# Kernel optimization log

Measured on AMD Instinct MI355X. Metric: run time of the kernel, lower is better.

The kernel has to match this reference:

```python
import jax, jax.numpy as jnp
import numpy as np

THRESHOLD = 0.9
EPS = 1e-12


def setup_inputs() -> dict:
    key = jax.random.key(0)
    ks = jax.random.split(key, 7)
    B, D_in, H1, H2, D_out = 8192, 256, 512, 256, 64
    # torch Linear default init ~ U(-1/sqrt(fan_in), 1/sqrt(fan_in)); randn scaled is fine as a stand-in
    def lin(k, out_f, in_f):
        return jax.random.normal(k, (out_f, in_f), dtype=jnp.float32) / np.sqrt(in_f)
    return {
        "x": jax.random.normal(ks[0], (B, D_in), dtype=jnp.float32),
        "W1": lin(ks[1], H1, D_in),
        "b1": jax.random.normal(ks[2], (H1,), dtype=jnp.float32) * 0.01,
        "W2": lin(ks[3], H2, H1),
        "b2": jax.random.normal(ks[4], (H2,), dtype=jnp.float32) * 0.01,
        "W3": lin(ks[5], D_out, H2),
        "b3": jax.random.normal(ks[6], (D_out,), dtype=jnp.float32) * 0.01,
    }


def reference(x, W1, b1, W2, b2, W3, b3):
    # MLP: Linear -> Tanh -> Linear -> Tanh -> Linear (no tanh on last)
    h1 = jnp.tanh(x @ W1.T + b1)          # [B, 512]
    h2 = jnp.tanh(h1 @ W2.T + b2)         # [B, 256]
    out = h2 @ W3.T + b3                  # [B, 64]

    # Pairwise state fidelity: (normalized dot)^2, thresholded adjacency (diag excluded)
    norms = jnp.linalg.norm(out, axis=-1, keepdims=True)  # [B, 1]
    normed = out / (norms + EPS)
    fid = (normed @ normed.T) ** 2                         # [B, B]
    adj = (fid >= THRESHOLD).astype(out.dtype)
    B = out.shape[0]
    adj = adj * (1.0 - jnp.eye(B, dtype=out.dtype))        # no self-edges (i < j pairs only)

    return adj @ out                                       # [B, 64]
```

## Files before the change

### kernel.cpp

```cpp
#include <hip/hip_runtime.h>
#include <hip/hip_bf16.h>
#include <math.h>

#define B_ROWS 8192
#define D_IN   256
#define H1_DIM 512
#define H2_DIM 256
#define D_OUT  64
#define EPSF   1e-12f
#define THRESH 0.9f
#define BAND_LO 0.89f
#define BAND_HI 0.91f

typedef __attribute__((ext_vector_type(8))) short short8;
typedef __attribute__((ext_vector_type(4))) float f32x4;

__device__ inline float tanh_fast(float xx) {
  const float ax = fabsf(xx);
  const float t = __expf(-2.0f * ax);
  const float r = (1.0f - t) / (1.0f + t);
  return xx < 0.0f ? -r : r;
}

__device__ inline void splitf8(float4 a, float4 b, short8& h, short8& m) {
  float v[8] = {a.x, a.y, a.z, a.w, b.x, b.y, b.z, b.w};
  short h8[8], m8[8];
#pragma unroll
  for (int e = 0; e < 8; ++e) {
    __hip_bfloat16 hb = __float2bfloat16(v[e]);
    float hf = __bfloat162float(hb);
    __hip_bfloat16 mb = __float2bfloat16(v[e] - hf);
    h8[e] = *(short*)&hb;
    m8[e] = *(short*)&mb;
  }
  h = *(short8*)h8;
  m = *(short8*)m8;
}

__device__ inline void rd8_swz(const float* buf, int S, int row, int kl,
                               float4& a, float4& b) {
  const int xr = (row & 7) << 2;
  a = *(const float4*)&buf[(row * S + kl) ^ xr];
  b = *(const float4*)&buf[(row * S + kl + 4) ^ xr];
}

__device__ inline void pack8(const float* __restrict__ src, short* __restrict__ dh,
                             short* __restrict__ dm, int t, int C, int lgq) {
  const int lane = t & 63;
  const int g = t >> 6;
  const int q = g & ((1 << lgq) - 1);
  const int I = g >> lgq;
  const int row = I * 16 + (lane & 15);
  const int k0 = q * 32 + ((lane >> 4) << 3);
  const float* p = src + (size_t)row * C + k0;
  short8 hh, mm;
  splitf8(*(const float4*)p, *(const float4*)(p + 4), hh, mm);
  *(short8*)(dh + (size_t)t * 8) = hh;
  *(short8*)(dm + (size_t)t * 8) = mm;
}

__global__ __launch_bounds__(256)
void wpack(const float* __restrict__ W1, const float* __restrict__ W2,
           const float* __restrict__ W3,
           short* w1h, short* w1m, short* w2h, short* w2m,
           short* w3h, short* w3m) {
  const int b = blockIdx.x, tid = threadIdx.x;
  if (b < 64)        pack8(W1, w1h, w1m, b * 256 + tid, 256, 3);
  else if (b < 128)  pack8(W2, w2h, w2m, (b - 64) * 256 + tid, 512, 4);
  else               pack8(W3, w3h, w3m, (b - 128) * 256 + tid, 256, 3);
}

__global__ __launch_bounds__(512, 4)
void fused_mlp16(const float* __restrict__ x,
                 const short* __restrict__ w1h, const short* __restrict__ w1m,
                 const float* __restrict__ b1,
                 const short* __restrict__ w2h, const short* __restrict__ w2m,
                 const float* __restrict__ b2,
                 const short* __restrict__ w3h, const short* __restrict__ w3m,
                 const float* __restrict__ b3,
                 float* __restrict__ out, short* __restrict__ vph,
                 short* __restrict__ vpm, float* __restrict__ res) {
  __shared__ __align__(16) char smem[49152];
  short* xph   = (short*)smem;
  short* xpm   = (short*)(smem + 8192);
  float* wbuf1 = (float*)smem;
  float* wbuf3 = (float*)smem;
  short* h1h   = (short*)(smem + 16384);
  short* h1m   = (short*)(smem + 32768);
  float* wbuf2 = (float*)(smem + 16384);
  short* h2ph  = (short*)(smem + 32768);
  short* h2pm  = (short*)(smem + 40960);
  __shared__ float nsum[16];
  __shared__ float invn[16];

  const int tid = threadIdx.x;
  const int wave = tid >> 6, lane = tid & 63;
  const int r0 = blockIdx.x * 16;
  const int col16 = lane & 15;
  const int rbase = (lane >> 4) << 2;

  if (tid < 256) {
    float4* rz = (float4*)(res + (size_t)r0 * D_OUT);
    rz[tid] = make_float4(0.f, 0.f, 0.f, 0.f);
  }

  {
    const int lu = tid & 63, q = tid >> 6;
    const float* p = x + (size_t)(r0 + (lu & 15)) * D_IN + q * 32 + ((lu >> 4) << 3);
    short8 hh, mm;
    splitf8(*(const float4*)p, *(const float4*)(p + 4), hh, mm);
    const int off = (q * 64 + lu) * 8;
    *(short8*)(xph + off) = hh;
    *(short8*)(xpm + off) = mm;
  }
  __syncthreads();

  f32x4 acc1[4];
#pragma unroll
  for (int jj = 0; jj < 4; ++jj) acc1[jj] = (f32x4){0.f, 0.f, 0.f, 0.f};
#pragma unroll 4
  for (int q = 0; q < 8; ++q) {
    const int aoff = (q * 64 + lane) * 8;
    const short8 Ah = *(const short8*)(xph + aoff);
    const short8 Am = *(const short8*)(xpm + aoff);
#pragma unroll
    for (int jj = 0; jj < 4; ++jj) {
      const int boff = (((wave * 4 + jj) * 8 + q) * 64 + lane) * 8;
      const short8 Bh = *(const short8*)(w1h + boff);
      const short8 Bm = *(const short8*)(w1m + boff);
      acc1[jj] = __builtin_amdgcn_mfma_f32_16x16x32_bf16(Ah, Bh, acc1[jj], 0, 0, 0);
      acc1[jj] = __builtin_amdgcn_mfma_f32_16x16x32_bf16(Ah, Bm, acc1[jj], 0, 0, 0);
      acc1[jj] = __builtin_amdgcn_mfma_f32_16x16x32_bf16(Am, Bh, acc1[jj], 0, 0, 0);
    }
  }
  __syncthreads();

  float bv1[4];
#pragma unroll
  for (int jj = 0; jj < 4; ++jj) bv1[jj] = b1[(wave * 4 + jj) * 16 + col16];
#pragma unroll
  for (int h = 0; h < 2; ++h) {
    if ((wave >> 2) == h) {
#pragma unroll
      for (int jj = 0; jj < 4; ++jj)
#pragma unroll
        for (int r = 0; r < 4; ++r) {
          const int row = rbase + r;
          const int col = ((wave & 3) * 4 + jj) * 16 + col16;
          wbuf1[(row * 256 + col) ^ ((row & 7) << 2)] = tanh_fast(acc1[jj][r] + bv1[jj]);
        }
    }
    __syncthreads();
    {
      const int lu = tid & 63, ql = tid >> 6;
      const int row = lu & 15, kl = ql * 32 + ((lu >> 4) << 3);
      float4 a, b;
      rd8_swz(wbuf1, 256, row, kl, a, b);
      short8 hh, mm;
      splitf8(a, b, hh, mm);
      const int off = ((h * 8 + ql) * 64 + lu) * 8;
      *(short8*)(h1h + off) = hh;
      *(short8*)(h1m + off) = mm;
    }
    __syncthreads();
  }

  f32x4 acc2[2];
#pragma unroll
  for (int jj = 0; jj < 2; ++jj) acc2[jj] = (f32x4){0.f, 0.f, 0.f, 0.f};
#pragma unroll 4
  for (int q = 0; q < 16; ++q) {
    const int aoff = (q * 64 + lane) * 8;
    const short8 Ah = *(const short8*)(h1h + aoff);
    const short8 Am = *(const short8*)(h1m + aoff);
#pragma unroll
    for (int jj = 0; jj < 2; ++jj) {
      const int boff = (((wave * 2 + jj) * 16 + q) * 64 + lane) * 8;
      const short8 Bh = *(const short8*)(w2h + boff);
      const short8 Bm = *(const short8*)(w2m + boff);
      acc2[jj] = __builtin_amdgcn_mfma_f32_16x16x32_bf16(Ah, Bh, acc2[jj], 0, 0, 0);
      acc2[jj] = __builtin_amdgcn_mfma_f32_16x16x32_bf16(Ah, Bm, acc2[jj], 0, 0, 0);
      acc2[jj] = __builtin_amdgcn_mfma_f32_16x16x32_bf16(Am, Bh, acc2[jj], 0, 0, 0);
    }
  }
  __syncthreads();

  {
    float bv2[2];
#pragma unroll
    for (int jj = 0; jj < 2; ++jj) bv2[jj] = b2[(wave * 2 + jj) * 16 + col16];
#pragma unroll
    for (int jj = 0; jj < 2; ++jj)
#pragma unroll
      for (int r = 0; r < 4; ++r) {
        const int row = rbase + r;
        const int col = (wave * 2 + jj) * 16 + col16;
        wbuf2[(row * 256 + col) ^ ((row & 7) << 2)] = tanh_fast(acc2[jj][r] + bv2[jj]);
      }
  }
  __syncthreads();
  {
    const int lu = tid & 63, ql = tid >> 6;
    const int row = lu & 15, kl = ql * 32 + ((lu >> 4) << 3);
    float4 a, b;
    rd8_swz(wbuf2, 256, row, kl, a, b);
    short8 hh, mm;
    splitf8(a, b, hh, mm);
    const int off = (ql * 64 + lu) * 8;
    *(short8*)(h2ph + off) = hh;
    *(short8*)(h2pm + off) = mm;
  }
  __syncthreads();

  if (wave < 4) {
    f32x4 acc3 = (f32x4){0.f, 0.f, 0.f, 0.f};
#pragma unroll 4
    for (int q = 0; q < 8; ++q) {
      const int aoff = (q * 64 + lane) * 8;
      const short8 Ah = *(const short8*)(h2ph + aoff);
      const short8 Am = *(const short8*)(h2pm + aoff);
      const int boff = ((wave * 8 + q) * 64 + lane) * 8;
      const short8 Bh = *(const short8*)(w3h + boff);
      const short8 Bm = *(const short8*)(w3m + boff);
      acc3 = __builtin_amdgcn_mfma_f32_16x16x32_bf16(Ah, Bh, acc3, 0, 0, 0);
      acc3 = __builtin_amdgcn_mfma_f32_16x16x32_bf16(Ah, Bm, acc3, 0, 0, 0);
      acc3 = __builtin_amdgcn_mfma_f32_16x16x32_bf16(Am, Bh, acc3, 0, 0, 0);
    }
    const float bv3 = b3[wave * 16 + col16];
#pragma unroll
    for (int r = 0; r < 4; ++r) {
      const int row = rbase + r;
      const int col = wave * 16 + col16;
      wbuf3[(row * 64 + col) ^ ((row & 7) << 2)] = acc3[r] + bv3;
    }
  }
  __syncthreads();

  if (tid < 256) {
    const int row = tid >> 4, c4 = (tid & 15) * 4;
    const float4 a = *(const float4*)&wbuf3[(row * 64 + c4) ^ ((row & 7) << 2)];
    float s = a.x * a.x + a.y * a.y + a.z * a.z + a.w * a.w;
    s += __shfl_xor(s, 1, 64);
    s += __shfl_xor(s, 2, 64);
    s += __shfl_xor(s, 4, 64);
    s += __shfl_xor(s, 8, 64);
    if ((tid & 15) == 0) nsum[row] = s;
  }
  __syncthreads();
  if (tid < 16) invn[tid] = 1.0f / (sqrtf(nsum[tid]) + EPSF);
  __syncthreads();

  if (tid < 256) {
    const int row = tid >> 4, c4 = (tid & 15) * 4;
    *(float4*)(out + (size_t)(r0 + row) * D_OUT + c4) =
        *(const float4*)&wbuf3[(row * 64 + c4) ^ ((row & 7) << 2)];
  }
  if (tid < 128) {
    const int lu = tid & 63, ql = tid >> 6;
    const int row = lu & 15, kl = ql * 32 + ((lu >> 4) << 3);
    const float sc = invn[row];
    float4 a, b;
    rd8_swz(wbuf3, 64, row, kl, a, b);
    a.x *= sc; a.y *= sc; a.z *= sc; a.w *= sc;
    b.x *= sc; b.y *= sc; b.z *= sc; b.w *= sc;
    short8 hh, mm;
    splitf8(a, b, hh, mm);
    const size_t off = (((size_t)blockIdx.x * 2 + ql) * 64 + lu) * 8;
    *(short8*)(vph + off) = hh;
    *(short8*)(vpm + off) = mm;
  }
}

__global__ __launch_bounds__(256, 2)
void gram_accum(const short* __restrict__ vph, const short* __restrict__ vpm,
                const float* __restrict__ out, float* __restrict__ res) {
  __shared__ __align__(16) short lAh[8 * 1024];
  const int tid = threadIdx.x;
  const int wave = tid >> 6, lane = tid & 63;

  const int t = blockIdx.x;
  int I = (int)((129.0f - sqrtf(16641.0f - 8.0f * (float)t)) * 0.5f);
  if (I < 0) I = 0;
  while (64 * (I + 1) - ((I + 1) * I) / 2 <= t) ++I;
  while (64 * I - (I * (I - 1)) / 2 > t) --I;
  const int Jc = I + (t - (64 * I - (I * (I - 1)) / 2));
  const int i0 = I * 128;
  const int j0c = Jc * 128;

  {
    const size_t base = (size_t)I * 8192;
#pragma unroll
    for (int u = 0; u < 4; ++u) {
      const int item = wave * 4 + u;
      __builtin_amdgcn_global_load_lds(
          (const __attribute__((address_space(1))) void*)(vph + base + item * 512 + lane * 8),
          (__attribute__((address_space(3))) void*)(lAh + item * 512), 16, 0, 0);
    }
  }
  __syncthreads();

  short8 Ah[8][2];
#pragma unroll
  for (int it = 0; it < 8; ++it)
#pragma unroll
    for (int q = 0; q < 2; ++q)
      Ah[it][q] = *(const short8*)(lAh + it * 1024 + q * 512 + lane * 8);

#pragma unroll
  for (int tt = 0; tt < 2; ++tt) {
    const int jt = wave * 2 + tt;
    const int j0 = j0c + jt * 16;
    const short* jb_h = vph + (size_t)(j0 >> 4) * 1024;
    short8 Bh0 = *(const short8*)(jb_h + lane * 8);
    short8 Bh1 = *(const short8*)(jb_h + 512 + lane * 8);

    f32x4 g[8];
#pragma unroll
    for (int it = 0; it < 8; ++it) g[it] = (f32x4){0.f, 0.f, 0.f, 0.f};
#pragma unroll
    for (int it = 0; it < 8; ++it) g[it] = __builtin_amdgcn_mfma_f32_16x16x32_bf16(Ah[it][0], Bh0, g[it], 0, 0, 0);
#pragma unroll
    for (int it = 0; it < 8; ++it) g[it] = __builtin_amdgcn_mfma_f32_16x16x32_bf16(Ah[it][1], Bh1, g[it], 0, 0, 0);

    bool band = false;
#pragma unroll
    for (int it = 0; it < 8; ++it)
#pragma unroll
      for (int r = 0; r < 4; ++r) {
        const float f = g[it][r] * g[it][r];
        band = band || (f > BAND_LO && f < BAND_HI);
      }
    if (__any(band)) {
      const short* jb_m = vpm + (size_t)(j0 >> 4) * 1024;
      short8 Bm0 = *(const short8*)(jb_m + lane * 8);
      short8 Bm1 = *(const short8*)(jb_m + 512 + lane * 8);
#pragma unroll
      for (int it = 0; it < 8; ++it) g[it] = __builtin_amdgcn_mfma_f32_16x16x32_bf16(Ah[it][0], Bm0, g[it], 0, 0, 0);
#pragma unroll
      for (int it = 0; it < 8; ++it) g[it] = __builtin_amdgcn_mfma_f32_16x16x32_bf16(Ah[it][1], Bm1, g[it], 0, 0, 0);
#pragma unroll
      for (int it = 0; it < 8; ++it) {
        const size_t abase = (size_t)((i0 >> 4) + it) * 1024;
        short8 Am0 = *(const short8*)(vpm + abase + lane * 8);
        short8 Am1 = *(const short8*)(vpm + abase + 512 + lane * 8);
        g[it] = __builtin_amdgcn_mfma_f32_16x16x32_bf16(Am0, Bh0, g[it], 0, 0, 0);
        g[it] = __builtin_amdgcn_mfma_f32_16x16x32_bf16(Am1, Bh1, g[it], 0, 0, 0);
      }
    }

    const int jl = j0 + (lane & 15);
#pragma unroll
    for (int it = 0; it < 8; ++it)
#pragma unroll
      for (int r = 0; r < 4; ++r) {
        const int il = i0 + it * 16 + (lane >> 4) * 4 + r;
        unsigned long long m =
            __ballot((g[it][r] * g[it][r] >= THRESH) && (il < jl));
        while (m) {
          const int s = __builtin_ctzll(m);
          m &= m - 1;
          const int js = j0 + (s & 15);
          const int is = i0 + it * 16 + ((s >> 4) << 2) + r;
          atomicAdd(res + (size_t)is * D_OUT + lane, out[(size_t)js * D_OUT + lane]);
          atomicAdd(res + (size_t)js * D_OUT + lane, out[(size_t)is * D_OUT + lane]);
        }
      }
  }
}

#define MB (1024 * 1024)
#define KB 1024

extern "C" void kernel_launch(void* const* d_in, const int* in_sizes, int n_in,
                              void* d_out, int out_size, void* d_ws, size_t ws_size,
                              hipStream_t stream) {
  const float* x  = (const float*)d_in[0];
  const float* W1 = (const float*)d_in[1];
  const float* b1 = (const float*)d_in[2];
  const float* W2 = (const float*)d_in[3];
  const float* b2 = (const float*)d_in[4];
  const float* W3 = (const float*)d_in[5];
  const float* b3 = (const float*)d_in[6];
  float* res = (float*)d_out;

  char* ws = (char*)d_ws;
  float* out = (float*)(ws);
  short* vph = (short*)(ws + 2 * MB);
  short* vpm = (short*)(ws + 3 * MB);
  short* w1h = (short*)(ws + 4 * MB);
  short* w1m = (short*)(ws + 4 * MB + 256 * KB);
  short* w2h = (short*)(ws + 4 * MB + 512 * KB);
  short* w2m = (short*)(ws + 4 * MB + 768 * KB);
  short* w3h = (short*)(ws + 5 * MB);
  short* w3m = (short*)(ws + 5 * MB + 32 * KB);

  wpack<<<136, 256, 0, stream>>>(W1, W2, W3, w1h, w1m, w2h, w2m, w3h, w3m);
  fused_mlp16<<<512, 512, 0, stream>>>(x, w1h, w1m, b1, w2h, w2m, b2,
                                       w3h, w3m, b3, out, vph, vpm, res);
  gram_accum<<<dim3(2080), 256, 0, stream>>>(vph, vpm, out, res);
}
```

Baseline: 117.9 us.

## Process 32 rows per MLP block and stream Gram A-fragments from LDS

```diff
diff --git a/kernel.cpp b/kernel.cpp
--- a/kernel.cpp
+++ b/kernel.cpp
@@ -70,8 +70,8 @@
   else               pack8(W3, w3h, w3m, (b - 128) * 256 + tid, 256, 3);
 }
 
-__global__ __launch_bounds__(512, 4)
-void fused_mlp16(const float* __restrict__ x,
+__global__ __launch_bounds__(512, 2)
+void fused_mlp32(const float* __restrict__ x,
                  const short* __restrict__ w1h, const short* __restrict__ w1m,
                  const float* __restrict__ b1,
                  const short* __restrict__ w2h, const short* __restrict__ w2m,
@@ -80,57 +80,67 @@
                  const float* __restrict__ b3,
                  float* __restrict__ out, short* __restrict__ vph,
                  short* __restrict__ vpm, float* __restrict__ res) {
-  __shared__ __align__(16) char smem[49152];
+  __shared__ __align__(16) char smem[98304];
   short* xph   = (short*)smem;
-  short* xpm   = (short*)(smem + 8192);
-  float* wbuf1 = (float*)smem;
-  float* wbuf3 = (float*)smem;
-  short* h1h   = (short*)(smem + 16384);
-  short* h1m   = (short*)(smem + 32768);
-  float* wbuf2 = (float*)(smem + 16384);
+  short* xpm   = (short*)(smem + 16384);
+  float* wbuf  = (float*)smem;
+  short* h1h   = (short*)(smem + 32768);
+  short* h1m   = (short*)(smem + 65536);
   short* h2ph  = (short*)(smem + 32768);
-  short* h2pm  = (short*)(smem + 40960);
-  __shared__ float nsum[16];
-  __shared__ float invn[16];
+  short* h2pm  = (short*)(smem + 49152);
+  __shared__ float nsum[32];
+  __shared__ float invn[32];
 
   const int tid = threadIdx.x;
   const int wave = tid >> 6, lane = tid & 63;
-  const int r0 = blockIdx.x * 16;
+  const int r0 = blockIdx.x * 32;
   const int col16 = lane & 15;
   const int rbase = (lane >> 4) << 2;
 
-  if (tid < 256) {
+  {
     float4* rz = (float4*)(res + (size_t)r0 * D_OUT);
     rz[tid] = make_float4(0.f, 0.f, 0.f, 0.f);
   }
 
-  {
-    const int lu = tid & 63, q = tid >> 6;
-    const float* p = x + (size_t)(r0 + (lu & 15)) * D_IN + q * 32 + ((lu >> 4) << 3);
+#pragma unroll
+  for (int uu = 0; uu < 2; ++uu) {
+    const int u = tid + uu * 512;
+    const int lu = u & 63, g = u >> 6;
+    const int q = g & 7, it = g >> 3;
+    const float* p = x + (size_t)(r0 + it * 16 + (lu & 15)) * D_IN + q * 32 + ((lu >> 4) << 3);
     short8 hh, mm;
     splitf8(*(const float4*)p, *(const float4*)(p + 4), hh, mm);
-    const int off = (q * 64 + lu) * 8;
+    const int off = ((it * 8 + q) * 64 + lu) * 8;
     *(short8*)(xph + off) = hh;
     *(short8*)(xpm + off) = mm;
   }
   __syncthreads();
 
-  f32x4 acc1[4];
-#pragma unroll
-  for (int jj = 0; jj < 4; ++jj) acc1[jj] = (f32x4){0.f, 0.f, 0.f, 0.f};
-#pragma unroll 4
+  f32x4 acc1[2][4];
+#pragma unroll
+  for (int it = 0; it < 2; ++it)
+#pragma unroll
+    for (int jj = 0; jj < 4; ++jj) acc1[it][jj] = (f32x4){0.f, 0.f, 0.f, 0.f};
+#pragma unroll 2
   for (int q = 0; q < 8; ++q) {
-    const int aoff = (q * 64 + lane) * 8;
-    const short8 Ah = *(const short8*)(xph + aoff);
-    const short8 Am = *(const short8*)(xpm + aoff);
+    short8 Ah[2], Am[2];
+#pragma unroll
+    for (int it = 0; it < 2; ++it) {
+      const int aoff = ((it * 8 + q) * 64 + lane) * 8;
+      Ah[it] = *(const short8*)(xph + aoff);
+      Am[it] = *(const short8*)(xpm + aoff);
+    }
 #pragma unroll
     for (int jj = 0; jj < 4; ++jj) {
       const int boff = (((wave * 4 + jj) * 8 + q) * 64 + lane) * 8;
       const short8 Bh = *(const short8*)(w1h + boff);
       const short8 Bm = *(const short8*)(w1m + boff);
-      acc1[jj] = __builtin_amdgcn_mfma_f32_16x16x32_bf16(Ah, Bh, acc1[jj], 0, 0, 0);
-      acc1[jj] = __builtin_amdgcn_mfma_f32_16x16x32_bf16(Ah, Bm, acc1[jj], 0, 0, 0);
-      acc1[jj] = __builtin_amdgcn_mfma_f32_16x16x32_bf16(Am, Bh, acc1[jj], 0, 0, 0);
+#pragma unroll
+      for (int it = 0; it < 2; ++it) {
+        acc1[it][jj] = __builtin_amdgcn_mfma_f32_16x16x32_bf16(Ah[it], Bh, acc1[it][jj], 0, 0, 0);
+        acc1[it][jj] = __builtin_amdgcn_mfma_f32_16x16x32_bf16(Ah[it], Bm, acc1[it][jj], 0, 0, 0);
+        acc1[it][jj] = __builtin_amdgcn_mfma_f32_16x16x32_bf16(Am[it], Bh, acc1[it][jj], 0, 0, 0);
+      }
     }
   }
   __syncthreads();
@@ -142,103 +152,122 @@
   for (int h = 0; h < 2; ++h) {
     if ((wave >> 2) == h) {
 #pragma unroll
-      for (int jj = 0; jj < 4; ++jj)
-#pragma unroll
-        for (int r = 0; r < 4; ++r) {
-          const int row = rbase + r;
-          const int col = ((wave & 3) * 4 + jj) * 16 + col16;
-          wbuf1[(row * 256 + col) ^ ((row & 7) << 2)] = tanh_fast(acc1[jj][r] + bv1[jj]);
-        }
+      for (int it = 0; it < 2; ++it)
+#pragma unroll
+        for (int jj = 0; jj < 4; ++jj)
+#pragma unroll
+          for (int r = 0; r < 4; ++r) {
+            const int row = it * 16 + rbase + r;
+            const int col = ((wave & 3) * 4 + jj) * 16 + col16;
+            wbuf[(row * 256 + col) ^ ((row & 7) << 2)] = tanh_fast(acc1[it][jj][r] + bv1[jj]);
+          }
     }
     __syncthreads();
-    {
-      const int lu = tid & 63, ql = tid >> 6;
-      const int row = lu & 15, kl = ql * 32 + ((lu >> 4) << 3);
+#pragma unroll
+    for (int uu = 0; uu < 2; ++uu) {
+      const int u = tid + uu * 512;
+      const int lu = u & 63, g = u >> 6;
+      const int ql = g & 7, it = g >> 3;
+      const int row = it * 16 + (lu & 15), kl = ql * 32 + ((lu >> 4) << 3);
       float4 a, b;
-      rd8_swz(wbuf1, 256, row, kl, a, b);
+      rd8_swz(wbuf, 256, row, kl, a, b);
       short8 hh, mm;
       splitf8(a, b, hh, mm);
-      const int off = ((h * 8 + ql) * 64 + lu) * 8;
+      const int off = ((it * 16 + h * 8 + ql) * 64 + lu) * 8;
       *(short8*)(h1h + off) = hh;
       *(short8*)(h1m + off) = mm;
     }
     __syncthreads();
   }
 
-  f32x4 acc2[2];
-#pragma unroll
-  for (int jj = 0; jj < 2; ++jj) acc2[jj] = (f32x4){0.f, 0.f, 0.f, 0.f};
-#pragma unroll 4
+  f32x4 acc2[2][2];
+#pragma unroll
+  for (int it = 0; it < 2; ++it)
+#pragma unroll
+    for (int jj = 0; jj < 2; ++jj) acc2[it][jj] = (f32x4){0.f, 0.f, 0.f, 0.f};
+#pragma unroll 2
   for (int q = 0; q < 16; ++q) {
-    const int aoff = (q * 64 + lane) * 8;
-    const short8 Ah = *(const short8*)(h1h + aoff);
-    const short8 Am = *(const short8*)(h1m + aoff);
+    short8 Ah[2], Am[2];
+#pragma unroll
+    for (int it = 0; it < 2; ++it) {
+      const int aoff = ((it * 16 + q) * 64 + lane) * 8;
+      Ah[it] = *(const short8*)(h1h + aoff);
+      Am[it] = *(const short8*)(h1m + aoff);
+    }
 #pragma unroll
     for (int jj = 0; jj < 2; ++jj) {
       const int boff = (((wave * 2 + jj) * 16 + q) * 64 + lane) * 8;
       const short8 Bh = *(const short8*)(w2h + boff);
       const short8 Bm = *(const short8*)(w2m + boff);
-      acc2[jj] = __builtin_amdgcn_mfma_f32_16x16x32_bf16(Ah, Bh, acc2[jj], 0, 0, 0);
-      acc2[jj] = __builtin_amdgcn_mfma_f32_16x16x32_bf16(Ah, Bm, acc2[jj], 0, 0, 0);
-      acc2[jj] = __builtin_amdgcn_mfma_f32_16x16x32_bf16(Am, Bh, acc2[jj], 0, 0, 0);
-    }
-  }
-  __syncthreads();
+#pragma unroll
+      for (int it = 0; it < 2; ++it) {
+        acc2[it][jj] = __builtin_amdgcn_mfma_f32_16x16x32_bf16(Ah[it], Bh, acc2[it][jj], 0, 0, 0);
+        acc2[it][jj] = __builtin_amdgcn_mfma_f32_16x16x32_bf16(Ah[it], Bm, acc2[it][jj], 0, 0, 0);
+        acc2[it][jj] = __builtin_amdgcn_mfma_f32_16x16x32_bf16(Am[it], Bh, acc2[it][jj], 0, 0, 0);
+      }
+    }
+  }
 
   {
     float bv2[2];
 #pragma unroll
     for (int jj = 0; jj < 2; ++jj) bv2[jj] = b2[(wave * 2 + jj) * 16 + col16];
 #pragma unroll
-    for (int jj = 0; jj < 2; ++jj)
-#pragma unroll
-      for (int r = 0; r < 4; ++r) {
-        const int row = rbase + r;
-        const int col = (wave * 2 + jj) * 16 + col16;
-        wbuf2[(row * 256 + col) ^ ((row & 7) << 2)] = tanh_fast(acc2[jj][r] + bv2[jj]);
-      }
-  }
-  __syncthreads();
-  {
-    const int lu = tid & 63, ql = tid >> 6;
-    const int row = lu & 15, kl = ql * 32 + ((lu >> 4) << 3);
+    for (int it = 0; it < 2; ++it)
+#pragma unroll
+      for (int jj = 0; jj < 2; ++jj)
+#pragma unroll
+        for (int r = 0; r < 4; ++r) {
+          const int row = it * 16 + rbase + r;
+          const int col = (wave * 2 + jj) * 16 + col16;
+          wbuf[(row * 256 + col) ^ ((row & 7) << 2)] = tanh_fast(acc2[it][jj][r] + bv2[jj]);
+        }
+  }
+  __syncthreads();
+#pragma unroll
+  for (int uu = 0; uu < 2; ++uu) {
+    const int u = tid + uu * 512;
+    const int lu = u & 63, g = u >> 6;
+    const int ql = g & 7, it = g >> 3;
+    const int row = it * 16 + (lu & 15), kl = ql * 32 + ((lu >> 4) << 3);
     float4 a, b;
-    rd8_swz(wbuf2, 256, row, kl, a, b);
+    rd8_swz(wbuf, 256, row, kl, a, b);
     short8 hh, mm;
     splitf8(a, b, hh, mm);
-    const int off = (ql * 64 + lu) * 8;
+    const int off = ((it * 8 + ql) * 64 + lu) * 8;
     *(short8*)(h2ph + off) = hh;
     *(short8*)(h2pm + off) = mm;
   }
   __syncthreads();
 
-  if (wave < 4) {
+  {
+    const int it = wave >> 2, jt = wave & 3;
     f32x4 acc3 = (f32x4){0.f, 0.f, 0.f, 0.f};
-#pragma unroll 4
+#pragma unroll 2
     for (int q = 0; q < 8; ++q) {
-      const int aoff = (q * 64 + lane) * 8;
+      const int aoff = ((it * 8 + q) * 64 + lane) * 8;
       const short8 Ah = *(const short8*)(h2ph + aoff);
       const short8 Am = *(const short8*)(h2pm + aoff);
-      const int boff = ((wave * 8 + q) * 64 + lane) * 8;
+      const int boff = ((jt * 8 + q) * 64 + lane) * 8;
       const short8 Bh = *(const short8*)(w3h + boff);
       const short8 Bm = *(const short8*)(w3m + boff);
       acc3 = __builtin_amdgcn_mfma_f32_16x16x32_bf16(Ah, Bh, acc3, 0, 0, 0);
       acc3 = __builtin_amdgcn_mfma_f32_16x16x32_bf16(Ah, Bm, acc3, 0, 0, 0);
       acc3 = __builtin_amdgcn_mfma_f32_16x16x32_bf16(Am, Bh, acc3, 0, 0, 0);
     }
-    const float bv3 = b3[wave * 16 + col16];
+    const float bv3 = b3[jt * 16 + col16];
 #pragma unroll
     for (int r = 0; r < 4; ++r) {
-      const int row = rbase + r;
-      const int col = wave * 16 + col16;
-      wbuf3[(row * 64 + col) ^ ((row & 7) << 2)] = acc3[r] + bv3;
-    }
-  }
-  __syncthreads();
-
-  if (tid < 256) {
+      const int row = it * 16 + rbase + r;
+      const int col = jt * 16 + col16;
+      wbuf[(row * 64 + col) ^ ((row & 7) << 2)] = acc3[r] + bv3;
+    }
+  }
+  __syncthreads();
+
+  {
     const int row = tid >> 4, c4 = (tid & 15) * 4;
-    const float4 a = *(const float4*)&wbuf3[(row * 64 + c4) ^ ((row & 7) << 2)];
+    const float4 a = *(const float4*)&wbuf[(row * 64 + c4) ^ ((row & 7) << 2)];
     float s = a.x * a.x + a.y * a.y + a.z * a.z + a.w * a.w;
     s += __shfl_xor(s, 1, 64);
     s += __shfl_xor(s, 2, 64);
@@ -247,31 +276,32 @@
     if ((tid & 15) == 0) nsum[row] = s;
   }
   __syncthreads();
-  if (tid < 16) invn[tid] = 1.0f / (sqrtf(nsum[tid]) + EPSF);
-  __syncthreads();
-
-  if (tid < 256) {
+  if (tid < 32) invn[tid] = 1.0f / (sqrtf(nsum[tid]) + EPSF);
+  __syncthreads();
+
+  {
     const int row = tid >> 4, c4 = (tid & 15) * 4;
     *(float4*)(out + (size_t)(r0 + row) * D_OUT + c4) =
-        *(const float4*)&wbuf3[(row * 64 + c4) ^ ((row & 7) << 2)];
-  }
-  if (tid < 128) {
-    const int lu = tid & 63, ql = tid >> 6;
-    const int row = lu & 15, kl = ql * 32 + ((lu >> 4) << 3);
+        *(const float4*)&wbuf[(row * 64 + c4) ^ ((row & 7) << 2)];
+  }
+  if (tid < 256) {
+    const int lu = tid & 63, g = tid >> 6;
+    const int ql = g & 1, it = g >> 1;
+    const int row = it * 16 + (lu & 15), kl = ql * 32 + ((lu >> 4) << 3);
     const float sc = invn[row];
     float4 a, b;
-    rd8_swz(wbuf3, 64, row, kl, a, b);
+    rd8_swz(wbuf, 64, row, kl, a, b);
     a.x *= sc; a.y *= sc; a.z *= sc; a.w *= sc;
     b.x *= sc; b.y *= sc; b.z *= sc; b.w *= sc;
     short8 hh, mm;
     splitf8(a, b, hh, mm);
-    const size_t off = (((size_t)blockIdx.x * 2 + ql) * 64 + lu) * 8;
+    const size_t off = (((size_t)(blockIdx.x * 2 + it) * 2 + ql) * 64 + lu) * 8;
     *(short8*)(vph + off) = hh;
     *(short8*)(vpm + off) = mm;
   }
 }
 
-__global__ __launch_bounds__(256, 2)
+__global__ __launch_bounds__(256, 4)
 void gram_accum(const short* __restrict__ vph, const short* __restrict__ vpm,
                 const float* __restrict__ out, float* __restrict__ res) {
   __shared__ __align__(16) short lAh[8 * 1024];
@@ -299,13 +329,6 @@
   }
   __syncthreads();
 
-  short8 Ah[8][2];
-#pragma unroll
-  for (int it = 0; it < 8; ++it)
-#pragma unroll
-    for (int q = 0; q < 2; ++q)
-      Ah[it][q] = *(const short8*)(lAh + it * 1024 + q * 512 + lane * 8);
-
 #pragma unroll
   for (int tt = 0; tt < 2; ++tt) {
     const int jt = wave * 2 + tt;
@@ -318,9 +341,15 @@
 #pragma unroll
     for (int it = 0; it < 8; ++it) g[it] = (f32x4){0.f, 0.f, 0.f, 0.f};
 #pragma unroll
-    for (int it = 0; it < 8; ++it) g[it] = __builtin_amdgcn_mfma_f32_16x16x32_bf16(Ah[it][0], Bh0, g[it], 0, 0, 0);
-#pragma unroll
-    for (int it = 0; it < 8; ++it) g[it] = __builtin_amdgcn_mfma_f32_16x16x32_bf16(Ah[it][1], Bh1, g[it], 0, 0, 0);
+    for (int it = 0; it < 8; ++it) {
+      const short8 A0 = *(const short8*)(lAh + it * 1024 + lane * 8);
+      g[it] = __builtin_amdgcn_mfma_f32_16x16x32_bf16(A0, Bh0, g[it], 0, 0, 0);
+    }
+#pragma unroll
+    for (int it = 0; it < 8; ++it) {
+      const short8 A1 = *(const short8*)(lAh + it * 1024 + 512 + lane * 8);
+      g[it] = __builtin_amdgcn_mfma_f32_16x16x32_bf16(A1, Bh1, g[it], 0, 0, 0);
+    }
 
     bool band = false;
 #pragma unroll
@@ -335,14 +364,14 @@
       short8 Bm0 = *(const short8*)(jb_m + lane * 8);
       short8 Bm1 = *(const short8*)(jb_m + 512 + lane * 8);
 #pragma unroll
-      for (int it = 0; it < 8; ++it) g[it] = __builtin_amdgcn_mfma_f32_16x16x32_bf16(Ah[it][0], Bm0, g[it], 0, 0, 0);
-#pragma unroll
-      for (int it = 0; it < 8; ++it) g[it] = __builtin_amdgcn_mfma_f32_16x16x32_bf16(Ah[it][1], Bm1, g[it], 0, 0, 0);
-#pragma unroll
       for (int it = 0; it < 8; ++it) {
+        const short8 A0 = *(const short8*)(lAh + it * 1024 + lane * 8);
+        const short8 A1 = *(const short8*)(lAh + it * 1024 + 512 + lane * 8);
+        g[it] = __builtin_amdgcn_mfma_f32_16x16x32_bf16(A0, Bm0, g[it], 0, 0, 0);
+        g[it] = __builtin_amdgcn_mfma_f32_16x16x32_bf16(A1, Bm1, g[it], 0, 0, 0);
         const size_t abase = (size_t)((i0 >> 4) + it) * 1024;
-        short8 Am0 = *(const short8*)(vpm + abase + lane * 8);
-        short8 Am1 = *(const short8*)(vpm + abase + 512 + lane * 8);
+        const short8 Am0 = *(const short8*)(vpm + abase + lane * 8);
+        const short8 Am1 = *(const short8*)(vpm + abase + 512 + lane * 8);
         g[it] = __builtin_amdgcn_mfma_f32_16x16x32_bf16(Am0, Bh0, g[it], 0, 0, 0);
         g[it] = __builtin_amdgcn_mfma_f32_16x16x32_bf16(Am1, Bh1, g[it], 0, 0, 0);
       }
@@ -395,7 +424,7 @@
   short* w3m = (short*)(ws + 5 * MB + 32 * KB);
 
   wpack<<<136, 256, 0, stream>>>(W1, W2, W3, w1h, w1m, w2h, w2m, w3h, w3m);
-  fused_mlp16<<<512, 512, 0, stream>>>(x, w1h, w1m, b1, w2h, w2m, b2,
+  fused_mlp32<<<256, 512, 0, stream>>>(x, w1h, w1m, b1, w2h, w2m, b2,
                                        w3h, w3m, b3, out, vph, vpm, res);
   gram_accum<<<dim3(2080), 256, 0, stream>>>(vph, vpm, out, res);
 }
```

Measured after the change: 138.6 us. 17.6% more time.

## Replace atomic scatter with adjacency bitmap plus per-row gather-sum kernel

Applied to the files above, without the earlier changes.

```diff
diff --git a/kernel.cpp b/kernel.cpp
--- a/kernel.cpp
+++ b/kernel.cpp
@@ -79,7 +79,7 @@
                  const short* __restrict__ w3h, const short* __restrict__ w3m,
                  const float* __restrict__ b3,
                  float* __restrict__ out, short* __restrict__ vph,
-                 short* __restrict__ vpm, float* __restrict__ res) {
+                 short* __restrict__ vpm) {
   __shared__ __align__(16) char smem[49152];
   short* xph   = (short*)smem;
   short* xpm   = (short*)(smem + 8192);
@@ -98,11 +98,6 @@
   const int r0 = blockIdx.x * 16;
   const int col16 = lane & 15;
   const int rbase = (lane >> 4) << 2;
-
-  if (tid < 256) {
-    float4* rz = (float4*)(res + (size_t)r0 * D_OUT);
-    rz[tid] = make_float4(0.f, 0.f, 0.f, 0.f);
-  }
 
   {
     const int lu = tid & 63, q = tid >> 6;
@@ -271,10 +266,12 @@
   }
 }
 
-__global__ __launch_bounds__(256, 2)
-void gram_accum(const short* __restrict__ vph, const short* __restrict__ vpm,
-                const float* __restrict__ out, float* __restrict__ res) {
+__global__ __launch_bounds__(256, 4)
+void gram_bits(const short* __restrict__ vph, const short* __restrict__ vpm,
+               unsigned short* __restrict__ bm) {
   __shared__ __align__(16) short lAh[8 * 1024];
+  __shared__ __align__(16) unsigned short ci[128 * 8];
+  __shared__ __align__(16) unsigned short cj[128 * 8];
   const int tid = threadIdx.x;
   const int wave = tid >> 6, lane = tid & 63;
 
@@ -299,12 +296,7 @@
   }
   __syncthreads();
 
-  short8 Ah[8][2];
-#pragma unroll
-  for (int it = 0; it < 8; ++it)
-#pragma unroll
-    for (int q = 0; q < 2; ++q)
-      Ah[it][q] = *(const short8*)(lAh + it * 1024 + q * 512 + lane * 8);
+  const int jloc = lane & 15;
 
 #pragma unroll
   for (int tt = 0; tt < 2; ++tt) {
@@ -318,9 +310,15 @@
 #pragma unroll
     for (int it = 0; it < 8; ++it) g[it] = (f32x4){0.f, 0.f, 0.f, 0.f};
 #pragma unroll
-    for (int it = 0; it < 8; ++it) g[it] = __builtin_amdgcn_mfma_f32_16x16x32_bf16(Ah[it][0], Bh0, g[it], 0, 0, 0);
-#pragma unroll
-    for (int it = 0; it < 8; ++it) g[it] = __builtin_amdgcn_mfma_f32_16x16x32_bf16(Ah[it][1], Bh1, g[it], 0, 0, 0);
+    for (int it = 0; it < 8; ++it) {
+      const short8 A0 = *(const short8*)(lAh + it * 1024 + lane * 8);
+      g[it] = __builtin_amdgcn_mfma_f32_16x16x32_bf16(A0, Bh0, g[it], 0, 0, 0);
+    }
+#pragma unroll
+    for (int it = 0; it < 8; ++it) {
+      const short8 A1 = *(const short8*)(lAh + it * 1024 + 512 + lane * 8);
+      g[it] = __builtin_amdgcn_mfma_f32_16x16x32_bf16(A1, Bh1, g[it], 0, 0, 0);
+    }
 
     bool band = false;
 #pragma unroll
@@ -335,37 +333,76 @@
       short8 Bm0 = *(const short8*)(jb_m + lane * 8);
       short8 Bm1 = *(const short8*)(jb_m + 512 + lane * 8);
 #pragma unroll
-      for (int it = 0; it < 8; ++it) g[it] = __builtin_amdgcn_mfma_f32_16x16x32_bf16(Ah[it][0], Bm0, g[it], 0, 0, 0);
-#pragma unroll
-      for (int it = 0; it < 8; ++it) g[it] = __builtin_amdgcn_mfma_f32_16x16x32_bf16(Ah[it][1], Bm1, g[it], 0, 0, 0);
-#pragma unroll
       for (int it = 0; it < 8; ++it) {
+        const short8 A0 = *(const short8*)(lAh + it * 1024 + lane * 8);
+        const short8 A1 = *(const short8*)(lAh + it * 1024 + 512 + lane * 8);
+        g[it] = __builtin_amdgcn_mfma_f32_16x16x32_bf16(A0, Bm0, g[it], 0, 0, 0);
+        g[it] = __builtin_amdgcn_mfma_f32_16x16x32_bf16(A1, Bm1, g[it], 0, 0, 0);
         const size_t abase = (size_t)((i0 >> 4) + it) * 1024;
-        short8 Am0 = *(const short8*)(vpm + abase + lane * 8);
-        short8 Am1 = *(const short8*)(vpm + abase + 512 + lane * 8);
+        const short8 Am0 = *(const short8*)(vpm + abase + lane * 8);
+        const short8 Am1 = *(const short8*)(vpm + abase + 512 + lane * 8);
         g[it] = __builtin_amdgcn_mfma_f32_16x16x32_bf16(Am0, Bh0, g[it], 0, 0, 0);
         g[it] = __builtin_amdgcn_mfma_f32_16x16x32_bf16(Am1, Bh1, g[it], 0, 0, 0);
       }
     }
 
-    const int jl = j0 + (lane & 15);
-#pragma unroll
-    for (int it = 0; it < 8; ++it)
+    const int jl = j0 + jloc;
+#pragma unroll
+    for (int it = 0; it < 8; ++it) {
+      unsigned int t16 = 0;
 #pragma unroll
       for (int r = 0; r < 4; ++r) {
         const int il = i0 + it * 16 + (lane >> 4) * 4 + r;
-        unsigned long long m =
-            __ballot((g[it][r] * g[it][r] >= THRESH) && (il < jl));
-        while (m) {
-          const int s = __builtin_ctzll(m);
-          m &= m - 1;
-          const int js = j0 + (s & 15);
-          const int is = i0 + it * 16 + ((s >> 4) << 2) + r;
-          atomicAdd(res + (size_t)is * D_OUT + lane, out[(size_t)js * D_OUT + lane]);
-          atomicAdd(res + (size_t)js * D_OUT + lane, out[(size_t)is * D_OUT + lane]);
-        }
+        const unsigned long long m =
+            __ballot((g[it][r] * g[it][r] >= THRESH) && (il != jl));
+        if (lane < 4)
+          ci[(it * 16 + lane * 4 + r) * 8 + jt] =
+              (unsigned short)((m >> (lane * 16)) & 0xFFFFu);
+        t16 |= ((unsigned int)((m >> jloc) & 1ull)) << r;
+        t16 |= ((unsigned int)((m >> (16 + jloc)) & 1ull)) << (4 + r);
+        t16 |= ((unsigned int)((m >> (32 + jloc)) & 1ull)) << (8 + r);
+        t16 |= ((unsigned int)((m >> (48 + jloc)) & 1ull)) << (12 + r);
       }
-  }
+      if (lane < 16) cj[(jt * 16 + jloc) * 8 + it] = (unsigned short)t16;
+    }
+  }
+  __syncthreads();
+
+  if (tid < 128) {
+    const uint4 v = *(const uint4*)&ci[tid * 8];
+    *(uint4*)((char*)bm + (size_t)(i0 + tid) * 1024 + (size_t)Jc * 16) = v;
+  } else if (I != Jc) {
+    const int lj = tid - 128;
+    const uint4 v = *(const uint4*)&cj[lj * 8];
+    *(uint4*)((char*)bm + (size_t)(j0c + lj) * 1024 + (size_t)I * 16) = v;
+  }
+}
+
+__global__ __launch_bounds__(256, 8)
+void bitsum(const ulonglong2* __restrict__ bm, const float* __restrict__ out,
+            float* __restrict__ res) {
+  const int wave = threadIdx.x >> 6, lane = threadIdx.x & 63;
+  const int row = blockIdx.x * 4 + wave;
+  const ulonglong2* rw = bm + (size_t)row * 64;
+  float acc = 0.f;
+  for (int w = 0; w < 64; ++w) {
+    ulonglong2 v = rw[w];
+    unsigned long long word = v.x;
+    int jb = w * 128;
+    while (word) {
+      const int b = __builtin_ctzll(word);
+      word &= word - 1;
+      acc += out[(size_t)(jb + b) * D_OUT + lane];
+    }
+    word = v.y;
+    jb += 64;
+    while (word) {
+      const int b = __builtin_ctzll(word);
+      word &= word - 1;
+      acc += out[(size_t)(jb + b) * D_OUT + lane];
+    }
+  }
+  res[(size_t)row * D_OUT + lane] = acc;
 }
 
 #define MB (1024 * 1024)
@@ -393,9 +430,11 @@
   short* w2m = (short*)(ws + 4 * MB + 768 * KB);
   short* w3h = (short*)(ws + 5 * MB);
   short* w3m = (short*)(ws + 5 * MB + 32 * KB);
+  unsigned short* bmap = (unsigned short*)(ws + 6 * MB);
 
   wpack<<<136, 256, 0, stream>>>(W1, W2, W3, w1h, w1m, w2h, w2m, w3h, w3m);
   fused_mlp16<<<512, 512, 0, stream>>>(x, w1h, w1m, b1, w2h, w2m, b2,
-                                       w3h, w3m, b3, out, vph, vpm, res);
-  gram_accum<<<dim3(2080), 256, 0, stream>>>(vph, vpm, out, res);
-}
+                                       w3h, w3m, b3, out, vph, vpm);
+  gram_bits<<<dim3(2080), 256, 0, stream>>>(vph, vpm, bmap);
+  bitsum<<<dim3(B_ROWS / 4), 256, 0, stream>>>((const ulonglong2*)bmap, out, res);
+}
```

After: 150.7 us. +27.8%, slower.

## Replace symmetric triangular gram tiles with full row-slab tiles accumulating in LDS

Applied to the files above, without the earlier changes.

```diff
diff --git a/kernel.cpp b/kernel.cpp
--- a/kernel.cpp
+++ b/kernel.cpp
@@ -79,7 +79,7 @@
                  const short* __restrict__ w3h, const short* __restrict__ w3m,
                  const float* __restrict__ b3,
                  float* __restrict__ out, short* __restrict__ vph,
-                 short* __restrict__ vpm, float* __restrict__ res) {
+                 short* __restrict__ vpm) {
   __shared__ __align__(16) char smem[49152];
   short* xph   = (short*)smem;
   short* xpm   = (short*)(smem + 8192);
@@ -98,11 +98,6 @@
   const int r0 = blockIdx.x * 16;
   const int col16 = lane & 15;
   const int rbase = (lane >> 4) << 2;
-
-  if (tid < 256) {
-    float4* rz = (float4*)(res + (size_t)r0 * D_OUT);
-    rz[tid] = make_float4(0.f, 0.f, 0.f, 0.f);
-  }
 
   {
     const int lu = tid & 63, q = tid >> 6;
@@ -272,20 +267,20 @@
 }
 
 __global__ __launch_bounds__(256, 2)
-void gram_accum(const short* __restrict__ vph, const short* __restrict__ vpm,
-                const float* __restrict__ out, float* __restrict__ res) {
+void gram_lds(const short* __restrict__ vph, const short* __restrict__ vpm,
+              const float* __restrict__ out, float* __restrict__ resp) {
   __shared__ __align__(16) short lAh[8 * 1024];
+  __shared__ __align__(16) float acc[128 * 64];
   const int tid = threadIdx.x;
   const int wave = tid >> 6, lane = tid & 63;
-
-  const int t = blockIdx.x;
-  int I = (int)((129.0f - sqrtf(16641.0f - 8.0f * (float)t)) * 0.5f);
-  if (I < 0) I = 0;
-  while (64 * (I + 1) - ((I + 1) * I) / 2 <= t) ++I;
-  while (64 * I - (I * (I - 1)) / 2 > t) --I;
-  const int Jc = I + (t - (64 * I - (I * (I - 1)) / 2));
+  const int I = blockIdx.x;
+  const int sl = blockIdx.y;
   const int i0 = I * 128;
-  const int j0c = Jc * 128;
+  const int jbase = sl * 1024;
+
+#pragma unroll
+  for (int u = 0; u < 8; ++u)
+    *(float4*)&acc[(u * 256 + tid) * 4] = make_float4(0.f, 0.f, 0.f, 0.f);
 
   {
     const size_t base = (size_t)I * 8192;
@@ -299,28 +294,26 @@
   }
   __syncthreads();
 
-  short8 Ah[8][2];
-#pragma unroll
-  for (int it = 0; it < 8; ++it)
-#pragma unroll
-    for (int q = 0; q < 2; ++q)
-      Ah[it][q] = *(const short8*)(lAh + it * 1024 + q * 512 + lane * 8);
-
-#pragma unroll
-  for (int tt = 0; tt < 2; ++tt) {
-    const int jt = wave * 2 + tt;
-    const int j0 = j0c + jt * 16;
+  for (int u = 0; u < 16; ++u) {
+    const int jt = u * 4 + wave;
+    const int j0 = jbase + jt * 16;
     const short* jb_h = vph + (size_t)(j0 >> 4) * 1024;
-    short8 Bh0 = *(const short8*)(jb_h + lane * 8);
-    short8 Bh1 = *(const short8*)(jb_h + 512 + lane * 8);
+    const short8 Bh0 = *(const short8*)(jb_h + lane * 8);
+    const short8 Bh1 = *(const short8*)(jb_h + 512 + lane * 8);
 
     f32x4 g[8];
 #pragma unroll
     for (int it = 0; it < 8; ++it) g[it] = (f32x4){0.f, 0.f, 0.f, 0.f};
 #pragma unroll
-    for (int it = 0; it < 8; ++it) g[it] = __builtin_amdgcn_mfma_f32_16x16x32_bf16(Ah[it][0], Bh0, g[it], 0, 0, 0);
-#pragma unroll
-    for (int it = 0; it < 8; ++it) g[it] = __builtin_amdgcn_mfma_f32_16x16x32_bf16(Ah[it][1], Bh1, g[it], 0, 0, 0);
+    for (int it = 0; it < 8; ++it) {
+      const short8 A0 = *(const short8*)(lAh + it * 1024 + lane * 8);
+      g[it] = __builtin_amdgcn_mfma_f32_16x16x32_bf16(A0, Bh0, g[it], 0, 0, 0);
+    }
+#pragma unroll
+    for (int it = 0; it < 8; ++it) {
+      const short8 A1 = *(const short8*)(lAh + it * 1024 + 512 + lane * 8);
+      g[it] = __builtin_amdgcn_mfma_f32_16x16x32_bf16(A1, Bh1, g[it], 0, 0, 0);
+    }
 
     bool band = false;
 #pragma unroll
@@ -332,20 +325,31 @@
       }
     if (__any(band)) {
       const short* jb_m = vpm + (size_t)(j0 >> 4) * 1024;
-      short8 Bm0 = *(const short8*)(jb_m + lane * 8);
-      short8 Bm1 = *(const short8*)(jb_m + 512 + lane * 8);
-#pragma unroll
-      for (int it = 0; it < 8; ++it) g[it] = __builtin_amdgcn_mfma_f32_16x16x32_bf16(Ah[it][0], Bm0, g[it], 0, 0, 0);
-#pragma unroll
-      for (int it = 0; it < 8; ++it) g[it] = __builtin_amdgcn_mfma_f32_16x16x32_bf16(Ah[it][1], Bm1, g[it], 0, 0, 0);
+      const short8 Bm0 = *(const short8*)(jb_m + lane * 8);
+      const short8 Bm1 = *(const short8*)(jb_m + 512 + lane * 8);
+      f32x4 g2a[8], g2b[8];
 #pragma unroll
       for (int it = 0; it < 8; ++it) {
+        g2a[it] = (f32x4){0.f, 0.f, 0.f, 0.f};
+        g2b[it] = (f32x4){0.f, 0.f, 0.f, 0.f};
+      }
+#pragma unroll
+      for (int it = 0; it < 8; ++it) {
+        const short8 A0 = *(const short8*)(lAh + it * 1024 + lane * 8);
+        const short8 A1 = *(const short8*)(lAh + it * 1024 + 512 + lane * 8);
+        g2a[it] = __builtin_amdgcn_mfma_f32_16x16x32_bf16(A0, Bm0, g2a[it], 0, 0, 0);
+        g2a[it] = __builtin_amdgcn_mfma_f32_16x16x32_bf16(A1, Bm1, g2a[it], 0, 0, 0);
         const size_t abase = (size_t)((i0 >> 4) + it) * 1024;
-        short8 Am0 = *(const short8*)(vpm + abase + lane * 8);
-        short8 Am1 = *(const short8*)(vpm + abase + 512 + lane * 8);
-        g[it] = __builtin_amdgcn_mfma_f32_16x16x32_bf16(Am0, Bh0, g[it], 0, 0, 0);
-        g[it] = __builtin_amdgcn_mfma_f32_16x16x32_bf16(Am1, Bh1, g[it], 0, 0, 0);
+        const short8 Am0 = *(const short8*)(vpm + abase + lane * 8);
+        const short8 Am1 = *(const short8*)(vpm + abase + 512 + lane * 8);
+        g2b[it] = __builtin_amdgcn_mfma_f32_16x16x32_bf16(Am0, Bh0, g2b[it], 0, 0, 0);
+        g2b[it] = __builtin_amdgcn_mfma_f32_16x16x32_bf16(Am1, Bh1, g2b[it], 0, 0, 0);
       }
+#pragma unroll
+      for (int it = 0; it < 8; ++it)
+#pragma unroll
+        for (int r = 0; r < 4; ++r)
+          g[it][r] += (g2a[it][r] + g2b[it][r]);
     }
 
     const int jl = j0 + (lane & 15);
@@ -355,17 +359,45 @@
       for (int r = 0; r < 4; ++r) {
         const int il = i0 + it * 16 + (lane >> 4) * 4 + r;
         unsigned long long m =
-            __ballot((g[it][r] * g[it][r] >= THRESH) && (il < jl));
+            __ballot((g[it][r] * g[it][r] >= THRESH) && (il != jl));
         while (m) {
-          const int s = __builtin_ctzll(m);
-          m &= m - 1;
-          const int js = j0 + (s & 15);
-          const int is = i0 + it * 16 + ((s >> 4) << 2) + r;
-          atomicAdd(res + (size_t)is * D_OUT + lane, out[(size_t)js * D_OUT + lane]);
-          atomicAdd(res + (size_t)js * D_OUT + lane, out[(size_t)is * D_OUT + lane]);
+          const int s0 = __builtin_ctzll(m); m &= m - 1;
+          int s1 = -1, s2 = -1, s3 = -1;
+          if (m) { s1 = __builtin_ctzll(m); m &= m - 1; }
+          if (m) { s2 = __builtin_ctzll(m); m &= m - 1; }
+          if (m) { s3 = __builtin_ctzll(m); m &= m - 1; }
+          const float v0 = out[(size_t)(j0 + (s0 & 15)) * D_OUT + lane];
+          float v1 = 0.f, v2 = 0.f, v3 = 0.f;
+          if (s1 >= 0) v1 = out[(size_t)(j0 + (s1 & 15)) * D_OUT + lane];
+          if (s2 >= 0) v2 = out[(size_t)(j0 + (s2 & 15)) * D_OUT + lane];
+          if (s3 >= 0) v3 = out[(size_t)(j0 + (s3 & 15)) * D_OUT + lane];
+          atomicAdd(&acc[(it * 16 + ((s0 >> 4) << 2) + r) * 64 + lane], v0);
+          if (s1 >= 0) atomicAdd(&acc[(it * 16 + ((s1 >> 4) << 2) + r) * 64 + lane], v1);
+          if (s2 >= 0) atomicAdd(&acc[(it * 16 + ((s2 >> 4) << 2) + r) * 64 + lane], v2);
+          if (s3 >= 0) atomicAdd(&acc[(it * 16 + ((s3 >> 4) << 2) + r) * 64 + lane], v3);
         }
       }
   }
+  __syncthreads();
+
+  float* dst = resp + ((size_t)sl * B_ROWS + i0) * D_OUT;
+#pragma unroll
+  for (int u = 0; u < 8; ++u) {
+    const int e = u * 256 + tid;
+    *(float4*)&dst[e * 4] = *(const float4*)&acc[e * 4];
+  }
+}
+
+__global__ __launch_bounds__(256)
+void reduce8(const float4* __restrict__ resp, float4* __restrict__ res) {
+  const int idx = blockIdx.x * 256 + threadIdx.x;
+  float4 a = resp[idx];
+#pragma unroll
+  for (int s = 1; s < 8; ++s) {
+    const float4 b = resp[(size_t)s * (B_ROWS * D_OUT / 4) + idx];
+    a.x += b.x; a.y += b.y; a.z += b.z; a.w += b.w;
+  }
+  res[idx] = a;
 }
 
 #define MB (1024 * 1024)
@@ -393,9 +425,12 @@
   short* w2m = (short*)(ws + 4 * MB + 768 * KB);
   short* w3h = (short*)(ws + 5 * MB);
   short* w3m = (short*)(ws + 5 * MB + 32 * KB);
+  float* resp = (float*)(ws + 6 * MB);
 
   wpack<<<136, 256, 0, stream>>>(W1, W2, W3, w1h, w1m, w2h, w2m, w3h, w3m);
   fused_mlp16<<<512, 512, 0, stream>>>(x, w1h, w1m, b1, w2h, w2m, b2,
-                                       w3h, w3m, b3, out, vph, vpm, res);
-  gram_accum<<<dim3(2080), 256, 0, stream>>>(vph, vpm, out, res);
-}
+                                       w3h, w3m, b3, out, vph, vpm);
+  gram_lds<<<dim3(64, 8), 256, 0, stream>>>(vph, vpm, out, resp);
+  reduce8<<<dim3(B_ROWS * D_OUT / 4 / 256), 256, 0, stream>>>(
+      (const float4*)resp, (float4*)res);
+}
```

Result: slower. 145.5 us (+23.4%).
